# Kernel tuning notes

Measured on AMD Instinct MI355X. Metric: run time of the kernel, lower is better.

The kernel has to match this reference:

```python
import jax, jax.numpy as jnp
import numpy as np
import math

L = 4          # transformer layers
H = 4          # heads
D = 256        # model_dim
DK = 64        # d_k
DV = D // H    # d_v = 64
DFF = 4 * D    # 1024
MOVES = 14
VDIM = 2 * D   # value head hidden
PDIM = 2 * D   # policy head hidden
B = 128        # graphs
NPG = 512      # nodes per graph
N = B * NPG    # 65536 total nodes
D_PE = D // 2  # encoder d_model = 128
MAX_LEN = 2000
PE_N = 10000.0


def make_pe():
    pos = jnp.arange(MAX_LEN, dtype=jnp.float32)[:, None]
    div = jnp.exp(jnp.arange(0, D_PE, 2, dtype=jnp.float32) * (-math.log(PE_N) / D_PE))
    ang = pos * div                      # (MAX_LEN, D_PE/2)
    return jnp.stack([jnp.sin(ang), jnp.cos(ang)], axis=-1).reshape(MAX_LEN, D_PE)


def layernorm(x, g, b, eps=1e-5):
    mu = jnp.mean(x, axis=-1, keepdims=True)
    var = jnp.mean((x - mu) ** 2, axis=-1, keepdims=True)
    return (x - mu) * jax.lax.rsqrt(var + eps) * g + b


def setup_inputs() -> dict:
    key = jax.random.key(0)
    ks = jax.random.split(key, 24)
    s = 0.02
    inp = {
        # stacked per-layer params
        'wq': jax.random.normal(ks[0], (L, H, D, DK), jnp.float32) * s,
        'wk': jax.random.normal(ks[1], (L, H, 5, D, DK), jnp.float32) * s,
        'wv': jax.random.normal(ks[2], (L, H, 5, D, DV), jnp.float32) * s,
        'ffn_w1': jax.random.normal(ks[3], (L, D, DFF), jnp.float32) * s,
        'ffn_b1': jnp.zeros((L, DFF), jnp.float32),
        'ffn_w2': jax.random.normal(ks[4], (L, DFF, D), jnp.float32) * s,
        'ffn_b2': jnp.zeros((L, D), jnp.float32),
        'ln1_g': jnp.ones((L, D), jnp.float32),
        'ln1_b': jnp.zeros((L, D), jnp.float32),
        'ln2_g': jnp.ones((L, D), jnp.float32),
        'ln2_b': jnp.zeros((L, D), jnp.float32),
        # heads
        'vw1': jax.random.normal(ks[5], (D, VDIM), jnp.float32) * s,
        'vb1': jnp.zeros((VDIM,), jnp.float32),
        'vw2': jax.random.normal(ks[6], (VDIM, 1), jnp.float32) * s,
        'vb2': jnp.zeros((1,), jnp.float32),
        'pw1': jax.random.normal(ks[7], (D, PDIM), jnp.float32) * s,
        'pb1': jnp.zeros((PDIM,), jnp.float32),
        'pw2': jax.random.normal(ks[8], (PDIM, MOVES), jnp.float32) * s,
        'pb2': jnp.zeros((MOVES,), jnp.float32),
    }
    # dowker: each node appears twice (over flag 0, under flag 1); nodes are
    # consecutive per graph so row r belongs to graph r // (2*NPG).
    rows = jnp.arange(2 * N)
    inp['dowker'] = jnp.stack([rows // 2, rows % 2], axis=1).astype(jnp.int32)
    inp['ptr'] = (jnp.arange(B + 1) * NPG).astype(jnp.int32)
    inp['adjacency'] = jax.random.randint(ks[9], (N, 4), 0, N, jnp.int32)
    return inp


def reference(wq, wk, wv, ffn_w1, ffn_b1, ffn_w2, ffn_b2, ln1_g, ln1_b, ln2_g,
              ln2_b, vw1, vb1, vw2, vb2, pw1, pb1, pw2, pb2,
              dowker, ptr, adjacency):
    pe = make_pe()
    n2 = dowker.shape[0]
    n = n2 // 2
    counts = ptr[1:] - ptr[:-1]                               # nodes per graph
    # --- BatchPositionalEncoding ---
    shifts = jnp.repeat(ptr[:-1] * 2, counts * 2, total_repeat_length=n2)
    local_seq = jnp.arange(n2) - shifts
    pe_vecs = pe[local_seq]                                   # (2N, D_PE)
    flat_idx = dowker[:, 0] * 2 + dowker[:, 1]
    out_flat = jnp.zeros((n2, D_PE), pe_vecs.dtype).at[flat_idx].set(pe_vecs)
    x = out_flat.reshape(n, 2 * D_PE)                         # (N, D)
    # --- stacked KnotTransformerLayers ---
    scale = 1.0 / math.sqrt(DK)
    for l in range(L):
        xn = jnp.concatenate([x[:, None, :], x[adjacency]], axis=1)  # (N,5,D)
        Q = jnp.einsum('nd,hdk->hnk', x, wq[l])
        K = jnp.einsum('nrd,hrdk->hnrk', xn, wk[l])
        V = jnp.einsum('nrd,hrdv->hnrv', xn, wv[l])
        A = jnp.einsum('hnk,hnrk->hnr', Q, K) * scale
        A = jax.nn.softmax(A, axis=1)   # NOTE: faithful to source F.softmax(dim=1) (node axis)
        Z = jnp.einsum('hnr,hnrv->hnv', A, V)
        Z = jnp.transpose(Z, (1, 0, 2)).reshape(n, -1)        # (N, D)
        x = layernorm(x + Z, ln1_g[l], ln1_b[l])
        h = jax.nn.relu(x @ ffn_w1[l] + ffn_b1[l]) @ ffn_w2[l] + ffn_b2[l]
        x = layernorm(x + h, ln2_g[l], ln2_b[l])
    # --- heads ---
    nb = ptr.shape[0] - 1
    seg = jnp.repeat(jnp.arange(nb), counts, total_repeat_length=n)
    pooled = jax.ops.segment_sum(x, seg, num_segments=nb) / counts[:, None].astype(x.dtype)
    value = jnp.tanh(jax.nn.relu(pooled @ vw1 + vb1) @ vw2 + vb2)[:, 0]   # (B,)
    policy = jax.nn.relu(x @ pw1 + pb1) @ pw2 + pb2                        # (N, MOVES)
    return policy, value
```

## Files before the change

kernel.cpp:

```cpp
#include <hip/hip_runtime.h>
#include <hip/hip_bf16.h>


typedef __attribute__((ext_vector_type(8))) short short8;
typedef __attribute__((ext_vector_type(4))) float floatx4;
typedef __attribute__((ext_vector_type(4))) unsigned short ushort4v;

__device__ __forceinline__ float b2f(unsigned short u){
  unsigned int b = ((unsigned int)u) << 16;
  float f; __builtin_memcpy(&f, &b, 4); return f;
}
__device__ __forceinline__ unsigned short f2b(float f){
  unsigned int b; __builtin_memcpy(&b, &f, 4);
  b += 0x7fffu + ((b >> 16) & 1u);
  return (unsigned short)(b >> 16);
}
__device__ __forceinline__ float ldf(const void* p, long i, int isbf){
  return isbf ? b2f(((const unsigned short*)p)[i]) : ((const float*)p)[i];
}
__device__ __forceinline__ float waveSum(float v){
  #pragma unroll
  for (int o = 32; o; o >>= 1) v += __shfl_xor(v, o);
  return v;
}
__device__ __forceinline__ float waveMax(float v){
  #pragma unroll
  for (int o = 32; o; o >>= 1) v = fmaxf(v, __shfl_xor(v, o));
  return v;
}
__device__ __forceinline__ float blockSum(float v, float* red){
  int w = threadIdx.x >> 6, lane = threadIdx.x & 63;
  v = waveSum(v);
  __syncthreads();
  if (lane == 0) red[w] = v;
  __syncthreads();
  return red[0] + red[1] + red[2] + red[3];
}
__device__ __forceinline__ float blockMax(float v, float* red){
  int w = threadIdx.x >> 6, lane = threadIdx.x & 63;
  v = waveMax(v);
  __syncthreads();
  if (lane == 0) red[w] = v;
  __syncthreads();
  return fmaxf(fmaxf(red[0], red[1]), fmaxf(red[2], red[3]));
}

__global__ void k_probe(const unsigned int* __restrict__ g1, int* __restrict__ flag){
  if (threadIdx.x == 0 && blockIdx.x == 0)
    *flag = (g1[0] == 0x3F803F80u) ? 1 : 0;
}
__global__ void k_zero_out(unsigned short* __restrict__ o, long n){
  long i = (long)blockIdx.x * blockDim.x + threadIdx.x;
  if (i < n) o[i] = 0;
}

__global__ __launch_bounds__(256) void k_wt(
    const void* __restrict__ src, unsigned short* __restrict__ dst,
    int K, int P, long total8, const int* __restrict__ flagp)
{
  const int isbf = *flagp;
  const long tid = (long)blockIdx.x * 256 + threadIdx.x;
  if (tid >= total8) return;
  const long base = tid * 8;
  const long mk = base / K;
  const int k0 = (int)(base - mk * K);
  const long m = mk / P;
  const int p = (int)(mk - m * P);
  const long sb = m * (long)K * P;
  short8 v;
  #pragma unroll
  for (int j = 0; j < 8; j++)
    v[j] = (short)f2b(ldf(src, sb + (long)(k0 + j) * P + p, isbf));
  *(short8*)(dst + base) = v;
}
__global__ __launch_bounds__(256) void k_wt_att(
    const void* __restrict__ src, unsigned short* __restrict__ dst,
    int R, long total8, const int* __restrict__ flagp)
{
  const int isbf = *flagp;
  const long tid = (long)blockIdx.x * 256 + threadIdx.x;
  if (tid >= total8) return;
  const long flat = tid * 8;
  const int d0 = (int)(flat & 255);
  const long rest = flat >> 8;
  const int c = (int)(rest & 255);
  const long lr = rest >> 8;
  const int r = (int)(lr % R);
  const long l = lr / R;
  const int h = c >> 6, dk = c & 63;
  const long sb = (((l * 4 + h) * R + r) * 256) * 64;
  short8 v;
  #pragma unroll
  for (int j = 0; j < 8; j++)
    v[j] = (short)f2b(ldf(src, sb + (long)(d0 + j) * 64 + dk, isbf));
  *(short8*)(dst + flat) = v;
}

__global__ __launch_bounds__(128) void k_pe(
    const int* __restrict__ dowker, const int* __restrict__ ptr, int B,
    float* __restrict__ x, int xf32, unsigned short* __restrict__ xb)
{
  const int r = blockIdx.x;
  const int d = threadIdx.x;
  int lo = 0, hi = B;
  while (lo + 1 < hi){ int mid = (lo + hi) >> 1; if (2*ptr[mid] <= r) lo = mid; else hi = mid; }
  const int p = r - 2*ptr[lo];
  const int j = d >> 1;
  const float ang = (float)p * expf(-0.14391156832f * (float)j);
  const float val = (d & 1) ? cosf(ang) : sinf(ang);
  const int t2 = dowker[2*r] * 2 + dowker[2*r + 1];
  const long idx = (long)(t2 >> 1) * 256 + (t2 & 1) * 128 + d;
  if (xf32) x[idx] = val;
  xb[idx] = f2b(val);
}

__device__ __forceinline__ void stage_xfull(
    unsigned short* Xf, const unsigned short* xb, long srow, int t)
{
  const int row = t >> 2, ss = t & 3;
  #pragma unroll
  for (int i = 0; i < 8; i++){
    const int c = ss * 8 + i * 32;
    *(short8*)(Xf + row * 264 + c) = *(const short8*)(xb + srow * 256 + c);
  }
}
__device__ __forceinline__ void gemm_tile(
    floatx4 (&acc)[4][4], const unsigned short* Xf, const unsigned short* Wsrc,
    unsigned short* Ws, int t, int lane, int h)
{
  const int wr0 = t >> 2, wss = t & 3;
  for (int k0 = 0; k0 < 256; k0 += 32){
    #pragma unroll
    for (int i = 0; i < 4; i++){
      const int p = wr0 + i * 64;
      *(short8*)(Ws + p * 40 + wss * 8) =
          *(const short8*)(Wsrc + (long)p * 256 + k0 + wss * 8);
    }
    __syncthreads();
    short8 a[4], bfr[4];
    #pragma unroll
    for (int rt = 0; rt < 4; rt++)
      a[rt] = *(const short8*)(Xf + (rt * 16 + (lane & 15)) * 264 + k0 + (lane >> 4) * 8);
    #pragma unroll
    for (int ct = 0; ct < 4; ct++)
      bfr[ct] = *(const short8*)(Ws + (h * 64 + ct * 16 + (lane & 15)) * 40 + (lane >> 4) * 8);
    #pragma unroll
    for (int rt = 0; rt < 4; rt++)
      #pragma unroll
      for (int ct = 0; ct < 4; ct++)
        acc[rt][ct] = __builtin_amdgcn_mfma_f32_16x16x32_bf16(a[rt], bfr[ct], acc[rt][ct], 0, 0, 0);
    __syncthreads();
  }
}
__device__ __forceinline__ void ln_epi2(
    const unsigned short* Zs, float* x, const unsigned short* xbres, int xf32,
    long bm, const void* g, const void* bb, long ofs, int isbf,
    unsigned short* xbout)
{
  const int t = threadIdx.x;
  const int w = t >> 6, lane = t & 63;
  float gv[4], bv[4];
  #pragma unroll
  for (int k = 0; k < 4; k++){
    gv[k] = ldf(g, ofs + lane * 4 + k, isbf);
    bv[k] = ldf(bb, ofs + lane * 4 + k, isbf);
  }
  for (int rr = 0; rr < 16; rr++){
    const int row = w * 16 + rr;
    const long gr = bm + row;
    float v[4];
    const ushort4v zv = *(const ushort4v*)(Zs + row * 264 + lane * 4);
    if (xf32){
      const floatx4 xv = *(const floatx4*)(x + gr * 256 + lane * 4);
      #pragma unroll
      for (int k = 0; k < 4; k++) v[k] = xv[k] + b2f(zv[k]);
    } else {
      const ushort4v xv = *(const ushort4v*)(xbres + gr * 256 + lane * 4);
      #pragma unroll
      for (int k = 0; k < 4; k++) v[k] = b2f(xv[k]) + b2f(zv[k]);
    }
    float s1 = v[0] + v[1] + v[2] + v[3];
    float s2 = v[0]*v[0] + v[1]*v[1] + v[2]*v[2] + v[3]*v[3];
    s1 = waveSum(s1);
    s2 = waveSum(s2);
    const float mu = s1 * (1.f / 256.f);
    const float rs = rsqrtf(s2 * (1.f / 256.f) - mu * mu + 1e-5f);
    floatx4 y; ushort4v o;
    #pragma unroll
    for (int k = 0; k < 4; k++){
      y[k] = (v[k] - mu) * rs * gv[k] + bv[k];
      o[k] = f2b(y[k]);
    }
    if (xf32) *(floatx4*)(x + gr * 256 + lane * 4) = y;
    *(ushort4v*)(xbout + gr * 256 + lane * 4) = o;
  }
}

__global__ __launch_bounds__(256) void k_att(
    const unsigned short* __restrict__ xb, const int* __restrict__ adj,
    const unsigned short* __restrict__ WqTl,
    const unsigned short* __restrict__ WkTl,
    float* __restrict__ A)
{
  __shared__ __align__(16) unsigned short Xf[64 * 264];
  __shared__ __align__(16) unsigned short Ws[256 * 40];
  const int t = threadIdx.x;
  const long bm = (long)blockIdx.x * 64;
  const int h = t >> 6, lane = t & 63;
  floatx4 accQ[4][4], accK[4][4];
  #pragma unroll
  for (int i = 0; i < 4; i++)
    #pragma unroll
    for (int j = 0; j < 4; j++) accQ[i][j] = floatx4{0.f,0.f,0.f,0.f};

  stage_xfull(Xf, xb, bm + (t >> 2), t);
  gemm_tile(accQ, Xf, WqTl, Ws, t, lane, h);
  for (int r = 0; r < 5; r++){
    if (r){
      __syncthreads();
      stage_xfull(Xf, xb, adj[(bm + (t >> 2)) * 4 + (r - 1)], t);
      __syncthreads();
    }
    #pragma unroll
    for (int i = 0; i < 4; i++)
      #pragma unroll
      for (int j = 0; j < 4; j++) accK[i][j] = floatx4{0.f,0.f,0.f,0.f};
    gemm_tile(accK, Xf, WkTl + (long)r * 65536, Ws, t, lane, h);
    #pragma unroll
    for (int rt = 0; rt < 4; rt++)
      #pragma unroll
      for (int j = 0; j < 4; j++){
        float p = accQ[rt][0][j]*accK[rt][0][j] + accQ[rt][1][j]*accK[rt][1][j]
                + accQ[rt][2][j]*accK[rt][2][j] + accQ[rt][3][j]*accK[rt][3][j];
        p += __shfl_xor(p, 1); p += __shfl_xor(p, 2);
        p += __shfl_xor(p, 4); p += __shfl_xor(p, 8);
        if ((lane & 15) == 0)
          A[(bm + rt * 16 + (lane >> 4) * 4 + j) * 20 + h * 5 + r] = 0.125f * p;
      }
  }
}

__global__ __launch_bounds__(256) void k_red1(
    const float* __restrict__ A, float* __restrict__ pm, float* __restrict__ ps, int nchunk)
{
  __shared__ float red[4];
  const int hr = blockIdx.x;
  const long n = (long)blockIdx.y * 256 + threadIdx.x;
  const float a = A[n * 20 + hr];
  const float m = blockMax(a, red);
  const float e = expf(a - m);
  const float s = blockSum(e, red);
  if (threadIdx.x == 0){ pm[hr * nchunk + blockIdx.y] = m; ps[hr * nchunk + blockIdx.y] = s; }
}
__global__ __launch_bounds__(256) void k_red2(
    const float* __restrict__ pm, const float* __restrict__ ps, float* __restrict__ MS, int nchunk)
{
  __shared__ float red[4];
  const int hr = blockIdx.x; const int t = threadIdx.x;
  const float m = (t < nchunk) ? pm[hr * nchunk + t] : -3.4e38f;
  const float s = (t < nchunk) ? ps[hr * nchunk + t] : 0.f;
  const float M = blockMax(m, red);
  const float S = blockSum(s * expf(m - M), red);
  if (t == 0){ MS[hr * 2] = M; MS[hr * 2 + 1] = S; }
}

__global__ __launch_bounds__(256) void k_vz(
    const unsigned short* __restrict__ xb, const int* __restrict__ adj,
    const unsigned short* __restrict__ WvTl,
    const float* __restrict__ A, const float* __restrict__ MS,
    float* __restrict__ x, int xf32, unsigned short* __restrict__ xbout,
    const void* __restrict__ g, const void* __restrict__ bb, long ofs,
    const int* __restrict__ flagp)
{
  const int isbf = *flagp;
  __shared__ __align__(16) unsigned short Xf[64 * 264];
  __shared__ __align__(16) unsigned short Ws[256 * 40];
  const int t = threadIdx.x;
  const long bm = (long)blockIdx.x * 64;
  const int h = t >> 6, lane = t & 63;
  floatx4 accz[4][4], accV[4][4];
  #pragma unroll
  for (int i = 0; i < 4; i++)
    #pragma unroll
    for (int j = 0; j < 4; j++) accz[i][j] = floatx4{0.f,0.f,0.f,0.f};

  for (int r = 0; r < 5; r++){
    const long srow = r ? (long)adj[(bm + (t >> 2)) * 4 + (r - 1)] : bm + (t >> 2);
    if (r) __syncthreads();
    stage_xfull(Xf, xb, srow, t);
    __syncthreads();
    #pragma unroll
    for (int i = 0; i < 4; i++)
      #pragma unroll
      for (int j = 0; j < 4; j++) accV[i][j] = floatx4{0.f,0.f,0.f,0.f};
    gemm_tile(accV, Xf, WvTl + (long)r * 65536, Ws, t, lane, h);
    const int hr = h * 5 + r;
    const float M = MS[hr * 2], invS = 1.f / MS[hr * 2 + 1];
    #pragma unroll
    for (int rt = 0; rt < 4; rt++)
      #pragma unroll
      for (int j = 0; j < 4; j++){
        const float wgt = expf(A[(bm + rt * 16 + (lane >> 4) * 4 + j) * 20 + hr] - M) * invS;
        #pragma unroll
        for (int ct = 0; ct < 4; ct++) accz[rt][ct][j] += wgt * accV[rt][ct][j];
      }
  }
  __syncthreads();
  #pragma unroll
  for (int rt = 0; rt < 4; rt++)
    #pragma unroll
    for (int ct = 0; ct < 4; ct++)
      #pragma unroll
      for (int j = 0; j < 4; j++)
        Xf[(rt * 16 + (lane >> 4) * 4 + j) * 264 + h * 64 + ct * 16 + (lane & 15)]
            = f2b(accz[rt][ct][j]);
  __syncthreads();
  ln_epi2(Xf, x, xb, xf32, bm, g, bb, ofs, isbf, xbout);
}

__global__ __launch_bounds__(256) void k_ffn(
    const unsigned short* __restrict__ xb,
    const unsigned short* __restrict__ W1T, const void* __restrict__ b1, long b1o,
    const unsigned short* __restrict__ W2T, const void* __restrict__ b2p, long b2o,
    float* __restrict__ x, int xf32, unsigned short* __restrict__ xbout,
    const void* __restrict__ g, const void* __restrict__ bb, long ofs,
    const int* __restrict__ flagp)
{
  const int isbf = *flagp;
  __shared__ __align__(16) unsigned short Xb[64 * 264];
  __shared__ __align__(16) unsigned short hs[64 * 72];
  __shared__ __align__(16) unsigned short WsU[256 * 40];
  const int t = threadIdx.x;
  const long bm = (long)blockIdx.x * 64;
  const int w = t >> 6, lane = t & 63;
  const int sr = t >> 2, ss = t & 3;
  stage_xfull(Xb, xb, bm + sr, t);
  __syncthreads();
  floatx4 acc2[4][4];
  #pragma unroll
  for (int rb = 0; rb < 4; rb++)
    #pragma unroll
    for (int nt = 0; nt < 4; nt++) acc2[rb][nt] = floatx4{0.f,0.f,0.f,0.f};

  for (int ct = 0; ct < 16; ct++){
    floatx4 acc1[4];
    #pragma unroll
    for (int i = 0; i < 4; i++) acc1[i] = floatx4{0.f,0.f,0.f,0.f};
    for (int k0 = 0; k0 < 256; k0 += 32){
      *(short8*)(WsU + sr * 40 + ss * 8) =
          *(const short8*)(W1T + (long)(ct * 64 + sr) * 256 + k0 + ss * 8);
      __syncthreads();
      const short8 a = *(const short8*)(Xb + (w * 16 + (lane & 15)) * 264 + k0 + (lane >> 4) * 8);
      #pragma unroll
      for (int nt = 0; nt < 4; nt++){
        const short8 b = *(const short8*)(WsU + (nt * 16 + (lane & 15)) * 40 + (lane >> 4) * 8);
        acc1[nt] = __builtin_amdgcn_mfma_f32_16x16x32_bf16(a, b, acc1[nt], 0, 0, 0);
      }
      __syncthreads();
    }
    const int lrow = w * 16 + (lane >> 4) * 4;
    #pragma unroll
    for (int nt = 0; nt < 4; nt++){
      const int ch = (lane & 15) + nt * 16;
      const float bv = ldf(b1, b1o + ct * 64 + ch, isbf);
      #pragma unroll
      for (int j = 0; j < 4; j++)
        hs[(lrow + j) * 72 + ch] = f2b(fmaxf(acc1[nt][j] + bv, 0.f));
    }
    __syncthreads();
    #pragma unroll
    for (int kk = 0; kk < 2; kk++){
      #pragma unroll
      for (int i = 0; i < 4; i++){
        const int p = sr + i * 64;
        *(short8*)(WsU + p * 40 + ss * 8) =
            *(const short8*)(W2T + (long)p * 1024 + ct * 64 + kk * 32 + ss * 8);
      }
      __syncthreads();
      short8 bfr[4];
      #pragma unroll
      for (int nt = 0; nt < 4; nt++)
        bfr[nt] = *(const short8*)(WsU + (w * 64 + nt * 16 + (lane & 15)) * 40 + (lane >> 4) * 8);
      #pragma unroll
      for (int rb = 0; rb < 4; rb++){
        const short8 a2 = *(const short8*)(hs + (rb * 16 + (lane & 15)) * 72 + kk * 32 + (lane >> 4) * 8);
        #pragma unroll
        for (int nt = 0; nt < 4; nt++)
          acc2[rb][nt] = __builtin_amdgcn_mfma_f32_16x16x32_bf16(a2, bfr[nt], acc2[rb][nt], 0, 0, 0);
      }
      __syncthreads();
    }
  }
  #pragma unroll
  for (int rb = 0; rb < 4; rb++)
    #pragma unroll
    for (int nt = 0; nt < 4; nt++){
      const int col = w * 64 + nt * 16 + (lane & 15);
      const float bv = ldf(b2p, b2o + col, isbf);
      #pragma unroll
      for (int j = 0; j < 4; j++)
        Xb[(rb * 16 + (lane >> 4) * 4 + j) * 264 + col] = f2b(acc2[rb][nt][j] + bv);
    }
  __syncthreads();
  ln_epi2(Xb, x, xb, xf32, bm, g, bb, ofs, isbf, xbout);
}

__global__ __launch_bounds__(256) void k_policy(
    const unsigned short* __restrict__ xb,
    const unsigned short* __restrict__ P1T,
    const void* __restrict__ pb1,
    const void* __restrict__ pw2, const void* __restrict__ pb2,
    void* __restrict__ out, const int* __restrict__ flagp)
{
  const int isbf = *flagp;
  __shared__ __align__(16) unsigned short buf[64 * 264];
  __shared__ __align__(16) unsigned short hs[64 * 72];
  __shared__ __align__(16) unsigned short Ws[64 * 40];
  __shared__ float p2s[896];
  const int t = threadIdx.x;
  const long bm = (long)blockIdx.x * 64;
  const int w = t >> 6, lane = t & 63;
  const int sr = t >> 2, ss = t & 3;
  stage_xfull(buf, xb, bm + sr, t);
  __syncthreads();
  float accp[4] = {0.f, 0.f, 0.f, 0.f};
  for (int ct = 0; ct < 8; ct++){
    floatx4 acc1[4];
    #pragma unroll
    for (int i = 0; i < 4; i++) acc1[i] = floatx4{0.f,0.f,0.f,0.f};
    for (int k0 = 0; k0 < 256; k0 += 32){
      *(short8*)(Ws + sr * 40 + ss * 8) =
          *(const short8*)(P1T + (long)(ct * 64 + sr) * 256 + k0 + ss * 8);
      __syncthreads();
      const short8 a = *(const short8*)(buf + (w * 16 + (lane & 15)) * 264 + k0 + (lane >> 4) * 8);
      #pragma unroll
      for (int nt = 0; nt < 4; nt++){
        const short8 b = *(const short8*)(Ws + (nt * 16 + (lane & 15)) * 40 + (lane >> 4) * 8);
        acc1[nt] = __builtin_amdgcn_mfma_f32_16x16x32_bf16(a, b, acc1[nt], 0, 0, 0);
      }
      __syncthreads();
    }
    const int lrow = w * 16 + (lane >> 4) * 4;
    #pragma unroll
    for (int nt = 0; nt < 4; nt++){
      const int ch = (lane & 15) + nt * 16;
      const float bv = ldf(pb1, ct * 64 + ch, isbf);
      #pragma unroll
      for (int j = 0; j < 4; j++)
        hs[(lrow + j) * 72 + ch] = f2b(fmaxf(acc1[nt][j] + bv, 0.f));
    }
    for (int i = t; i < 896; i += 256) p2s[i] = ldf(pw2, (long)ct * 896 + i, isbf);
    __syncthreads();
    #pragma unroll
    for (int i = 0; i < 4; i++){
      const int pi = t + i * 256;
      if (pi < 896){
        const int row = pi / 14, m = pi - row * 14;
        float s = 0.f;
        for (int c = 0; c < 64; c++) s += b2f(hs[row * 72 + c]) * p2s[c * 14 + m];
        accp[i] += s;
      }
    }
    __syncthreads();
  }
  #pragma unroll
  for (int i = 0; i < 4; i++){
    const int pi = t + i * 256;
    if (pi < 896){
      const int row = pi / 14, m = pi - row * 14;
      const float v = accp[i] + ldf(pb2, m, isbf);
      const long n = bm + row;
      if (isbf) ((unsigned short*)out)[n * 14 + m] = f2b(v);
      else      ((float*)out)[n * 14 + m] = v;
    }
  }
}

__global__ __launch_bounds__(256) void k_pool(
    const float* __restrict__ x, int xf32, const unsigned short* __restrict__ xb,
    const int* __restrict__ ptr, float* __restrict__ pooled)
{
  const int gi = blockIdx.x; const int t = threadIdx.x;
  const int base = ptr[gi], cnt = ptr[gi + 1] - base;
  float s = 0.f;
  for (int i = 0; i < cnt; i++){
    const long idx = (long)(base + i) * 256 + t;
    s += xf32 ? x[idx] : b2f(xb[idx]);
  }
  pooled[gi * 256 + t] = s / (float)cnt;
}
__global__ __launch_bounds__(256) void k_value(
    const float* __restrict__ pooled,
    const void* __restrict__ vw1, const void* __restrict__ vb1,
    const void* __restrict__ vw2, const void* __restrict__ vb2,
    void* __restrict__ out, long outOfs, const int* __restrict__ flagp)
{
  const int isbf = *flagp;
  __shared__ float pr[256];
  __shared__ float red[4];
  const int gi = blockIdx.x; const int t = threadIdx.x;
  pr[t] = pooled[gi * 256 + t];
  __syncthreads();
  float part = 0.f;
  #pragma unroll
  for (int rep = 0; rep < 2; rep++){
    const int j = t + rep * 256;
    float a = ldf(vb1, j, isbf);
    for (int d = 0; d < 256; d++) a += pr[d] * ldf(vw1, (long)d * 512 + j, isbf);
    a = fmaxf(a, 0.f);
    part += a * ldf(vw2, j, isbf);
  }
  const float s = blockSum(part, red);
  if (t == 0){
    const float v = tanhf(s + ldf(vb2, 0, isbf));
    if (isbf) ((unsigned short*)out)[outOfs + gi] = f2b(v);
    else      ((float*)out)[outOfs + gi] = v;
  }
}

extern "C" void kernel_launch(void* const* d_in, const int* in_sizes, int n_in,
                              void* d_out, int out_size, void* d_ws, size_t ws_size,
                              hipStream_t stream)
{
  const void* wq  = d_in[0];  const void* wk  = d_in[1];  const void* wv  = d_in[2];
  const void* fw1 = d_in[3];  const void* fb1 = d_in[4];  const void* fw2 = d_in[5];
  const void* fb2 = d_in[6];
  const void* g1  = d_in[7];  const void* b1  = d_in[8];
  const void* g2  = d_in[9];  const void* b2  = d_in[10];
  const void* vw1 = d_in[11]; const void* vb1 = d_in[12];
  const void* vw2 = d_in[13]; const void* vb2 = d_in[14];
  const void* pw1 = d_in[15]; const void* pb1 = d_in[16];
  const void* pw2 = d_in[17]; const void* pb2 = d_in[18];
  const int* dowker = (const int*)d_in[19];
  const int* ptr    = (const int*)d_in[20];
  const int* adj    = (const int*)d_in[21];

  const int B = in_sizes[20] - 1;
  const int N = in_sizes[21] / 4;
  const int NCH = N / 256;

  auto al = [](size_t s){ return ((s + 255) / 256) * 256; };
  const size_t sz_flag = 256;
  const size_t sz_A    = al((size_t)N * 20 * 4);
  const size_t sz_pm   = al((size_t)20 * NCH * 4);
  const size_t sz_MS   = 256;
  const size_t sz_pool = al((size_t)B * 256 * 4);
  const size_t sz_wqT  = al((size_t)4 * 65536 * 2);
  const size_t sz_wkT  = al((size_t)20 * 65536 * 2);
  const size_t sz_w1T  = al((size_t)4 * 262144 * 2);
  const size_t sz_p1T  = al((size_t)131072 * 2);
  const size_t sz_xb   = al((size_t)N * 256 * 2);
  const size_t sz_x32  = al((size_t)N * 256 * 4);
  const size_t fixed = sz_flag + sz_A + 2 * sz_pm + sz_MS + sz_pool
                     + sz_wqT + 2 * sz_wkT + 2 * sz_w1T + sz_p1T + 2 * sz_xb;

  int xf32;
  if      (ws_size >= fixed + sz_x32) xf32 = 1;
  else if (ws_size >= fixed)          xf32 = 0;
  else {
    long n = (long)out_size;
    k_zero_out<<<dim3((unsigned)((n + 255) / 256)), 256, 0, stream>>>(
        (unsigned short*)d_out, n);
    return;
  }

  char* wsp = (char*)d_ws;
  auto carve = [&](size_t bytes) -> char* { char* p = wsp; wsp += bytes; return p; };
  int* flag            = (int*)carve(sz_flag);
  unsigned short* xbA  = (unsigned short*)carve(sz_xb);
  unsigned short* xbB  = (unsigned short*)carve(sz_xb);
  float* A             = (float*)carve(sz_A);
  float* pm            = (float*)carve(sz_pm);
  float* ps            = (float*)carve(sz_pm);
  float* MS            = (float*)carve(sz_MS);
  float* pooled        = (float*)carve(sz_pool);
  unsigned short* wqT  = (unsigned short*)carve(sz_wqT);
  unsigned short* wkT  = (unsigned short*)carve(sz_wkT);
  unsigned short* wvT  = (unsigned short*)carve(sz_wkT);
  unsigned short* w1T  = (unsigned short*)carve(sz_w1T);
  unsigned short* w2T  = (unsigned short*)carve(sz_w1T);
  unsigned short* p1T  = (unsigned short*)carve(sz_p1T);
  float* x             = xf32 ? (float*)carve(sz_x32) : nullptr;

  k_probe<<<1, 64, 0, stream>>>((const unsigned int*)g1, flag);
  k_wt_att<<<dim3(128), 256, 0, stream>>>(wq, wqT, 1, 32768, flag);
  k_wt_att<<<dim3(640), 256, 0, stream>>>(wk, wkT, 5, 163840, flag);
  k_wt_att<<<dim3(640), 256, 0, stream>>>(wv, wvT, 5, 163840, flag);
  k_wt<<<dim3(512), 256, 0, stream>>>(fw1, w1T, 256, 1024, 131072, flag);
  k_wt<<<dim3(512), 256, 0, stream>>>(fw2, w2T, 1024, 256, 131072, flag);
  k_wt<<<dim3(64),  256, 0, stream>>>(pw1, p1T, 256, 512, 16384, flag);

  k_pe<<<dim3(2 * N), 128, 0, stream>>>(dowker, ptr, B, x, xf32, xbA);

  const dim3 gBlk(N / 64);
  for (int l = 0; l < 4; l++){
    k_att<<<gBlk, 256, 0, stream>>>(xbA, adj,
        wqT + (long)l * 65536, wkT + (long)l * 327680, A);
    k_red1<<<dim3(20, NCH), 256, 0, stream>>>(A, pm, ps, NCH);
    k_red2<<<dim3(20), 256, 0, stream>>>(pm, ps, MS, NCH);
    k_vz<<<gBlk, 256, 0, stream>>>(xbA, adj, wvT + (long)l * 327680, A, MS,
        x, xf32, xbB, g1, b1, (long)l * 256, flag);
    k_ffn<<<gBlk, 256, 0, stream>>>(xbB,
        w1T + (long)l * 262144, fb1, (long)l * 1024,
        w2T + (long)l * 262144, fb2, (long)l * 256,
        x, xf32, xbA, g2, b2, (long)l * 256, flag);
  }

  k_pool<<<dim3(B), 256, 0, stream>>>(x, xf32, xbA, ptr, pooled);
  k_value<<<dim3(B), 256, 0, stream>>>(pooled, vw1, vb1, vw2, vb2,
                                       d_out, (long)N * 14, flag);
  k_policy<<<gBlk, 256, 0, stream>>>(xbA, p1T, pb1, pw2, pb2, d_out, flag);
}
```

Before: 2.572 ms.

## Read MFMA weight fragments directly from global memory and drop LDS weight staging

The attention, value, FFN and policy kernels no longer copy weight tiles into shared memory behind __syncthreads. Each lane now loads its bf16 B-fragments straight from global memory, relying on L1/L2 caching of the small weight matrices. The FFN and policy kernels are also reorganised so each wave owns 16 rows end to end. That replaces block-wide barriers with wave-local fences and keeps the input rows in registers. The goal is to remove barrier stalls and LDS traffic. The cost is more global or cache load instructions and higher register pressure (16 accumulators plus 8 cached A fragments), which could reduce occupancy.

```diff
diff --git a/kernel.cpp b/kernel.cpp
--- a/kernel.cpp
+++ b/kernel.cpp
@@ -124,34 +124,6 @@
     *(short8*)(Xf + row * 264 + c) = *(const short8*)(xb + srow * 256 + c);
   }
 }
-__device__ __forceinline__ void gemm_tile(
-    floatx4 (&acc)[4][4], const unsigned short* Xf, const unsigned short* Wsrc,
-    unsigned short* Ws, int t, int lane, int h)
-{
-  const int wr0 = t >> 2, wss = t & 3;
-  for (int k0 = 0; k0 < 256; k0 += 32){
-    #pragma unroll
-    for (int i = 0; i < 4; i++){
-      const int p = wr0 + i * 64;
-      *(short8*)(Ws + p * 40 + wss * 8) =
-          *(const short8*)(Wsrc + (long)p * 256 + k0 + wss * 8);
-    }
-    __syncthreads();
-    short8 a[4], bfr[4];
-    #pragma unroll
-    for (int rt = 0; rt < 4; rt++)
-      a[rt] = *(const short8*)(Xf + (rt * 16 + (lane & 15)) * 264 + k0 + (lane >> 4) * 8);
-    #pragma unroll
-    for (int ct = 0; ct < 4; ct++)
-      bfr[ct] = *(const short8*)(Ws + (h * 64 + ct * 16 + (lane & 15)) * 40 + (lane >> 4) * 8);
-    #pragma unroll
-    for (int rt = 0; rt < 4; rt++)
-      #pragma unroll
-      for (int ct = 0; ct < 4; ct++)
-        acc[rt][ct] = __builtin_amdgcn_mfma_f32_16x16x32_bf16(a[rt], bfr[ct], acc[rt][ct], 0, 0, 0);
-    __syncthreads();
-  }
-}
 __device__ __forceinline__ void ln_epi2(
     const unsigned short* Zs, float* x, const unsigned short* xbres, int xf32,
     long bm, const void* g, const void* bb, long ofs, int isbf,
@@ -203,10 +175,10 @@
     float* __restrict__ A)
 {
   __shared__ __align__(16) unsigned short Xf[64 * 264];
-  __shared__ __align__(16) unsigned short Ws[256 * 40];
   const int t = threadIdx.x;
   const long bm = (long)blockIdx.x * 64;
   const int h = t >> 6, lane = t & 63;
+  const long colofs = (long)(h * 64 + (lane & 15)) * 256 + (lane >> 4) * 8;
   floatx4 accQ[4][4], accK[4][4];
   #pragma unroll
   for (int i = 0; i < 4; i++)
@@ -214,7 +186,21 @@
     for (int j = 0; j < 4; j++) accQ[i][j] = floatx4{0.f,0.f,0.f,0.f};
 
   stage_xfull(Xf, xb, bm + (t >> 2), t);
-  gemm_tile(accQ, Xf, WqTl, Ws, t, lane, h);
+  __syncthreads();
+  #pragma unroll
+  for (int k0 = 0; k0 < 8; k0++){
+    short8 a[4];
+    #pragma unroll
+    for (int rt = 0; rt < 4; rt++)
+      a[rt] = *(const short8*)(Xf + (rt * 16 + (lane & 15)) * 264 + k0 * 32 + (lane >> 4) * 8);
+    #pragma unroll
+    for (int ct = 0; ct < 4; ct++){
+      const short8 b = *(const short8*)(WqTl + colofs + ct * 4096 + k0 * 32);
+      #pragma unroll
+      for (int rt = 0; rt < 4; rt++)
+        accQ[rt][ct] = __builtin_amdgcn_mfma_f32_16x16x32_bf16(a[rt], b, accQ[rt][ct], 0, 0, 0);
+    }
+  }
   for (int r = 0; r < 5; r++){
     if (r){
       __syncthreads();
@@ -225,7 +211,21 @@
     for (int i = 0; i < 4; i++)
       #pragma unroll
       for (int j = 0; j < 4; j++) accK[i][j] = floatx4{0.f,0.f,0.f,0.f};
-    gemm_tile(accK, Xf, WkTl + (long)r * 65536, Ws, t, lane, h);
+    const unsigned short* wb = WkTl + (long)r * 65536 + colofs;
+    #pragma unroll
+    for (int k0 = 0; k0 < 8; k0++){
+      short8 a[4];
+      #pragma unroll
+      for (int rt = 0; rt < 4; rt++)
+        a[rt] = *(const short8*)(Xf + (rt * 16 + (lane & 15)) * 264 + k0 * 32 + (lane >> 4) * 8);
+      #pragma unroll
+      for (int ct = 0; ct < 4; ct++){
+        const short8 b = *(const short8*)(wb + ct * 4096 + k0 * 32);
+        #pragma unroll
+        for (int rt = 0; rt < 4; rt++)
+          accK[rt][ct] = __builtin_amdgcn_mfma_f32_16x16x32_bf16(a[rt], b, accK[rt][ct], 0, 0, 0);
+      }
+    }
     #pragma unroll
     for (int rt = 0; rt < 4; rt++)
       #pragma unroll
@@ -274,10 +274,10 @@
 {
   const int isbf = *flagp;
   __shared__ __align__(16) unsigned short Xf[64 * 264];
-  __shared__ __align__(16) unsigned short Ws[256 * 40];
   const int t = threadIdx.x;
   const long bm = (long)blockIdx.x * 64;
   const int h = t >> 6, lane = t & 63;
+  const long colofs = (long)(h * 64 + (lane & 15)) * 256 + (lane >> 4) * 8;
   floatx4 accz[4][4], accV[4][4];
   #pragma unroll
   for (int i = 0; i < 4; i++)
@@ -293,7 +293,21 @@
     for (int i = 0; i < 4; i++)
       #pragma unroll
       for (int j = 0; j < 4; j++) accV[i][j] = floatx4{0.f,0.f,0.f,0.f};
-    gemm_tile(accV, Xf, WvTl + (long)r * 65536, Ws, t, lane, h);
+    const unsigned short* wb = WvTl + (long)r * 65536 + colofs;
+    #pragma unroll
+    for (int k0 = 0; k0 < 8; k0++){
+      short8 a[4];
+      #pragma unroll
+      for (int rt = 0; rt < 4; rt++)
+        a[rt] = *(const short8*)(Xf + (rt * 16 + (lane & 15)) * 264 + k0 * 32 + (lane >> 4) * 8);
+      #pragma unroll
+      for (int ct = 0; ct < 4; ct++){
+        const short8 b = *(const short8*)(wb + ct * 4096 + k0 * 32);
+        #pragma unroll
+        for (int rt = 0; rt < 4; rt++)
+          accV[rt][ct] = __builtin_amdgcn_mfma_f32_16x16x32_bf16(a[rt], b, accV[rt][ct], 0, 0, 0);
+      }
+    }
     const int hr = h * 5 + r;
     const float M = MS[hr * 2], invS = 1.f / MS[hr * 2 + 1];
     #pragma unroll
@@ -327,82 +341,63 @@
     const int* __restrict__ flagp)
 {
   const int isbf = *flagp;
-  __shared__ __align__(16) unsigned short Xb[64 * 264];
+  __shared__ __align__(16) unsigned short Zs[64 * 264];
   __shared__ __align__(16) unsigned short hs[64 * 72];
-  __shared__ __align__(16) unsigned short WsU[256 * 40];
   const int t = threadIdx.x;
   const long bm = (long)blockIdx.x * 64;
   const int w = t >> 6, lane = t & 63;
-  const int sr = t >> 2, ss = t & 3;
-  stage_xfull(Xb, xb, bm + sr, t);
-  __syncthreads();
-  floatx4 acc2[4][4];
-  #pragma unroll
-  for (int rb = 0; rb < 4; rb++)
-    #pragma unroll
-    for (int nt = 0; nt < 4; nt++) acc2[rb][nt] = floatx4{0.f,0.f,0.f,0.f};
-
+  const unsigned short* xrow = xb + (bm + w * 16 + (lane & 15)) * 256 + (lane >> 4) * 8;
+  short8 a_x[8];
+  #pragma unroll
+  for (int k0 = 0; k0 < 8; k0++) a_x[k0] = *(const short8*)(xrow + k0 * 32);
+  floatx4 acc2[16];
+  #pragma unroll
+  for (int i = 0; i < 16; i++) acc2[i] = floatx4{0.f,0.f,0.f,0.f};
+
+  const long w1ofs = (long)(lane & 15) * 256 + (lane >> 4) * 8;
+  const long w2ofs = (long)(lane & 15) * 1024 + (lane >> 4) * 8;
   for (int ct = 0; ct < 16; ct++){
     floatx4 acc1[4];
     #pragma unroll
     for (int i = 0; i < 4; i++) acc1[i] = floatx4{0.f,0.f,0.f,0.f};
-    for (int k0 = 0; k0 < 256; k0 += 32){
-      *(short8*)(WsU + sr * 40 + ss * 8) =
-          *(const short8*)(W1T + (long)(ct * 64 + sr) * 256 + k0 + ss * 8);
-      __syncthreads();
-      const short8 a = *(const short8*)(Xb + (w * 16 + (lane & 15)) * 264 + k0 + (lane >> 4) * 8);
+    #pragma unroll
+    for (int k0 = 0; k0 < 8; k0++){
       #pragma unroll
       for (int nt = 0; nt < 4; nt++){
-        const short8 b = *(const short8*)(WsU + (nt * 16 + (lane & 15)) * 40 + (lane >> 4) * 8);
-        acc1[nt] = __builtin_amdgcn_mfma_f32_16x16x32_bf16(a, b, acc1[nt], 0, 0, 0);
-      }
-      __syncthreads();
-    }
-    const int lrow = w * 16 + (lane >> 4) * 4;
+        const short8 b = *(const short8*)(W1T + (long)(ct * 64 + nt * 16) * 256 + w1ofs + k0 * 32);
+        acc1[nt] = __builtin_amdgcn_mfma_f32_16x16x32_bf16(a_x[k0], b, acc1[nt], 0, 0, 0);
+      }
+    }
     #pragma unroll
     for (int nt = 0; nt < 4; nt++){
       const int ch = (lane & 15) + nt * 16;
       const float bv = ldf(b1, b1o + ct * 64 + ch, isbf);
       #pragma unroll
       for (int j = 0; j < 4; j++)
-        hs[(lrow + j) * 72 + ch] = f2b(fmaxf(acc1[nt][j] + bv, 0.f));
-    }
-    __syncthreads();
+        hs[(w * 16 + (lane >> 4) * 4 + j) * 72 + ch] = f2b(fmaxf(acc1[nt][j] + bv, 0.f));
+    }
+    __threadfence_block();
     #pragma unroll
     for (int kk = 0; kk < 2; kk++){
-      #pragma unroll
-      for (int i = 0; i < 4; i++){
-        const int p = sr + i * 64;
-        *(short8*)(WsU + p * 40 + ss * 8) =
-            *(const short8*)(W2T + (long)p * 1024 + ct * 64 + kk * 32 + ss * 8);
-      }
-      __syncthreads();
-      short8 bfr[4];
-      #pragma unroll
-      for (int nt = 0; nt < 4; nt++)
-        bfr[nt] = *(const short8*)(WsU + (w * 64 + nt * 16 + (lane & 15)) * 40 + (lane >> 4) * 8);
-      #pragma unroll
-      for (int rb = 0; rb < 4; rb++){
-        const short8 a2 = *(const short8*)(hs + (rb * 16 + (lane & 15)) * 72 + kk * 32 + (lane >> 4) * 8);
-        #pragma unroll
-        for (int nt = 0; nt < 4; nt++)
-          acc2[rb][nt] = __builtin_amdgcn_mfma_f32_16x16x32_bf16(a2, bfr[nt], acc2[rb][nt], 0, 0, 0);
-      }
-      __syncthreads();
-    }
-  }
-  #pragma unroll
-  for (int rb = 0; rb < 4; rb++)
-    #pragma unroll
-    for (int nt = 0; nt < 4; nt++){
-      const int col = w * 64 + nt * 16 + (lane & 15);
-      const float bv = ldf(b2p, b2o + col, isbf);
-      #pragma unroll
-      for (int j = 0; j < 4; j++)
-        Xb[(rb * 16 + (lane >> 4) * 4 + j) * 264 + col] = f2b(acc2[rb][nt][j] + bv);
-    }
-  __syncthreads();
-  ln_epi2(Xb, x, xb, xf32, bm, g, bb, ofs, isbf, xbout);
+      const short8 a2 = *(const short8*)(hs + (w * 16 + (lane & 15)) * 72 + kk * 32 + (lane >> 4) * 8);
+      #pragma unroll
+      for (int pt = 0; pt < 16; pt++){
+        const short8 b2 = *(const short8*)(W2T + (long)(pt * 16) * 1024 + w2ofs + ct * 64 + kk * 32);
+        acc2[pt] = __builtin_amdgcn_mfma_f32_16x16x32_bf16(a2, b2, acc2[pt], 0, 0, 0);
+      }
+    }
+    __threadfence_block();
+  }
+  #pragma unroll
+  for (int pt = 0; pt < 16; pt++){
+    const int col = pt * 16 + (lane & 15);
+    const float bv = ldf(b2p, b2o + col, isbf);
+    #pragma unroll
+    for (int j = 0; j < 4; j++)
+      Zs[(w * 16 + (lane >> 4) * 4 + j) * 264 + col] = f2b(acc2[pt][j] + bv);
+  }
+  __threadfence_block();
+  ln_epi2(Zs, x, xb, xf32, bm, g, bb, ofs, isbf, xbout);
 }
 
 __global__ __launch_bounds__(256) void k_policy(
@@ -413,63 +408,60 @@
     void* __restrict__ out, const int* __restrict__ flagp)
 {
   const int isbf = *flagp;
-  __shared__ __align__(16) unsigned short buf[64 * 264];
   __shared__ __align__(16) unsigned short hs[64 * 72];
-  __shared__ __align__(16) unsigned short Ws[64 * 40];
-  __shared__ float p2s[896];
+  __shared__ float p2s[7168];
   const int t = threadIdx.x;
   const long bm = (long)blockIdx.x * 64;
   const int w = t >> 6, lane = t & 63;
-  const int sr = t >> 2, ss = t & 3;
-  stage_xfull(buf, xb, bm + sr, t);
+  for (int i = t; i < 7168; i += 256) p2s[i] = ldf(pw2, i, isbf);
+  const unsigned short* xrow = xb + (bm + w * 16 + (lane & 15)) * 256 + (lane >> 4) * 8;
+  short8 a_x[8];
+  #pragma unroll
+  for (int k0 = 0; k0 < 8; k0++) a_x[k0] = *(const short8*)(xrow + k0 * 32);
   __syncthreads();
   float accp[4] = {0.f, 0.f, 0.f, 0.f};
+  const long p1ofs = (long)(lane & 15) * 256 + (lane >> 4) * 8;
   for (int ct = 0; ct < 8; ct++){
     floatx4 acc1[4];
     #pragma unroll
     for (int i = 0; i < 4; i++) acc1[i] = floatx4{0.f,0.f,0.f,0.f};
-    for (int k0 = 0; k0 < 256; k0 += 32){
-      *(short8*)(Ws + sr * 40 + ss * 8) =
-          *(const short8*)(P1T + (long)(ct * 64 + sr) * 256 + k0 + ss * 8);
-      __syncthreads();
-      const short8 a = *(const short8*)(buf + (w * 16 + (lane & 15)) * 264 + k0 + (lane >> 4) * 8);
+    #pragma unroll
+    for (int k0 = 0; k0 < 8; k0++){
       #pragma unroll
       for (int nt = 0; nt < 4; nt++){
-        const short8 b = *(const short8*)(Ws + (nt * 16 + (lane & 15)) * 40 + (lane >> 4) * 8);
-        acc1[nt] = __builtin_amdgcn_mfma_f32_16x16x32_bf16(a, b, acc1[nt], 0, 0, 0);
-      }
-      __syncthreads();
-    }
-    const int lrow = w * 16 + (lane >> 4) * 4;
+        const short8 b = *(const short8*)(P1T + (long)(ct * 64 + nt * 16) * 256 + p1ofs + k0 * 32);
+        acc1[nt] = __builtin_amdgcn_mfma_f32_16x16x32_bf16(a_x[k0], b, acc1[nt], 0, 0, 0);
+      }
+    }
     #pragma unroll
     for (int nt = 0; nt < 4; nt++){
       const int ch = (lane & 15) + nt * 16;
       const float bv = ldf(pb1, ct * 64 + ch, isbf);
       #pragma unroll
       for (int j = 0; j < 4; j++)
-        hs[(lrow + j) * 72 + ch] = f2b(fmaxf(acc1[nt][j] + bv, 0.f));
-    }
-    for (int i = t; i < 896; i += 256) p2s[i] = ldf(pw2, (long)ct * 896 + i, isbf);
-    __syncthreads();
-    #pragma unroll
-    for (int i = 0; i < 4; i++){
-      const int pi = t + i * 256;
-      if (pi < 896){
-        const int row = pi / 14, m = pi - row * 14;
+        hs[(w * 16 + (lane >> 4) * 4 + j) * 72 + ch] = f2b(fmaxf(acc1[nt][j] + bv, 0.f));
+    }
+    __threadfence_block();
+    #pragma unroll
+    for (int ii = 0; ii < 4; ii++){
+      const int idx = lane + ii * 64;
+      if (idx < 224){
+        const int rl = idx / 14, m = idx - rl * 14;
         float s = 0.f;
-        for (int c = 0; c < 64; c++) s += b2f(hs[row * 72 + c]) * p2s[c * 14 + m];
-        accp[i] += s;
-      }
-    }
-    __syncthreads();
-  }
-  #pragma unroll
-  for (int i = 0; i < 4; i++){
-    const int pi = t + i * 256;
-    if (pi < 896){
-      const int row = pi / 14, m = pi - row * 14;
-      const float v = accp[i] + ldf(pb2, m, isbf);
-      const long n = bm + row;
+        for (int c = 0; c < 64; c++)
+          s += b2f(hs[(w * 16 + rl) * 72 + c]) * p2s[(ct * 64 + c) * 14 + m];
+        accp[ii] += s;
+      }
+    }
+    __threadfence_block();
+  }
+  #pragma unroll
+  for (int ii = 0; ii < 4; ii++){
+    const int idx = lane + ii * 64;
+    if (idx < 224){
+      const int rl = idx / 14, m = idx - rl * 14;
+      const float v = accp[ii] + ldf(pb2, m, isbf);
+      const long n = bm + w * 16 + rl;
       if (isbf) ((unsigned short*)out)[n * 14 + m] = f2b(v);
       else      ((float*)out)[n * 14 + m] = v;
     }
```

New measurement: 4.227 ms. 1.64x slower.
